# Kernel optimization log

Hardware: AMD Instinct MI355X
Metric: run time of the kernel (lower is better)

The kernel has to match this reference:

```python
import jax, jax.numpy as jnp
import numpy as np

B, S, V, E, H, MAX_OOVS = 32, 1024, 32000, 256, 512, 12
D2 = 2 * H + 100          # encoder feature dim after binary concat
IN = E + D2               # GRU input size


def setup_inputs() -> dict:
    key = jax.random.key(0)
    ks = jax.random.split(key, 18)
    sc = 0.02
    return {
        "input_idx": jax.random.randint(ks[0], (B,), 0, V),
        "encoded": jax.random.normal(ks[1], (B, S, 2 * H), jnp.float32),
        "encoded_idx": jax.random.randint(ks[2], (B, S), 0, V + MAX_OOVS),
        "prev_state": jax.random.normal(ks[3], (B, H), jnp.float32),
        "weighted": jax.random.normal(ks[4], (B, 1, D2), jnp.float32),
        "binary_vectors": jax.random.uniform(ks[5], (B, S, 1), jnp.float32),
        "order": 1,
        "embed_table": jax.random.normal(ks[6], (V, E), jnp.float32) * sc,
        "W_ih": jax.random.normal(ks[7], (3 * H, IN), jnp.float32) * sc,
        "b_ih": jax.random.normal(ks[8], (3 * H,), jnp.float32) * sc,
        "W_hh": jax.random.normal(ks[9], (3 * H, H), jnp.float32) * sc,
        "b_hh": jax.random.normal(ks[10], (3 * H,), jnp.float32) * sc,
        "Wo_w": jax.random.normal(ks[11], (V, H), jnp.float32) * sc,
        "Wo_b": jax.random.normal(ks[12], (V,), jnp.float32) * sc,
        "Wc_w": jax.random.normal(ks[13], (H, D2), jnp.float32) * sc,
        "Wc_b": jax.random.normal(ks[14], (H,), jnp.float32) * sc,
        "Ws_w": jax.random.normal(ks[15], (H, D2), jnp.float32) * sc,
        "Ws_b": jax.random.normal(ks[16], (H,), jnp.float32) * sc,
    }


def _gru_step(x, h, W_ih, b_ih, W_hh, b_hh):
    # torch nn.GRU single-step math
    gi = x @ W_ih.T + b_ih
    gh = h @ W_hh.T + b_hh
    i_r, i_z, i_n = jnp.split(gi, 3, axis=1)
    h_r, h_z, h_n = jnp.split(gh, 3, axis=1)
    r = jax.nn.sigmoid(i_r + h_r)
    z = jax.nn.sigmoid(i_z + h_z)
    n = jnp.tanh(i_n + r * h_n)
    return (1.0 - z) * n + z * h


def reference(input_idx, encoded, encoded_idx, prev_state, weighted,
              binary_vectors, order, embed_table, W_ih, b_ih, W_hh, b_hh,
              Wo_w, Wo_b, Wc_w, Wc_b, Ws_w, Ws_b):
    b, s = encoded.shape[0], encoded.shape[1]
    vocab = Wo_w.shape[0]
    # concat binary feature expanded to 100 channels -> (b, s, 2H+100)
    bin100 = jnp.broadcast_to(binary_vectors, (b, s, 100))
    enc = jnp.concatenate([encoded, bin100], axis=2)

    if order == 0:
        prev_state = enc[:, -1] @ Ws_w.T + Ws_b
        weighted = jnp.zeros((b, 1, enc.shape[2]), enc.dtype)

    emb = embed_table[input_idx][:, None, :]          # (b,1,E)
    x = jnp.concatenate([emb, weighted], axis=2)[:, 0]  # (b, IN)
    state = _gru_step(x, prev_state, W_ih, b_ih, W_hh, b_hh)  # (b,H)

    score_g = state @ Wo_w.T + Wo_b                   # (b, V)
    sc = jnp.tanh(enc @ Wc_w.T + Wc_b)                # (b, s, H)
    score_c = jnp.tanh(jnp.einsum('bsh,bh->bs', sc, state))
    score_c = score_c + jnp.where(encoded_idx == 0, -1000.0, 0.0).astype(score_c.dtype)

    probs = jax.nn.softmax(jnp.concatenate([score_g, score_c], axis=1), axis=1)
    prob_g = probs[:, :vocab]
    prob_c = probs[:, vocab:]
    prob_c_given = prob_c / jnp.sum(prob_c)           # faithful: scalar sum over all elems

    oovs = jnp.full((b, MAX_OOVS), 1e-4, probs.dtype)
    prob_g = jnp.concatenate([prob_g, oovs], axis=1)  # (b, V+OOV)

    # scatter-add copy probs into vocab space (same math as one_hot + bmm)
    rows = jnp.arange(b)[:, None]
    prob_c_to_g = jnp.zeros((b, vocab + MAX_OOVS), probs.dtype).at[rows, encoded_idx].add(prob_c)
    out = (prob_g + prob_c_to_g)[:, None, :]          # (b,1,V+OOV)

    idx_from = (encoded_idx == input_idx[:, None]).astype(probs.dtype)
    ssum = idx_from.sum(axis=1, keepdims=True)
    idx_from = jnp.where(ssum > 1, idx_from / ssum, idx_from)

    attn = prob_c_given * idx_from                    # (b, s)
    weighted_out = jnp.einsum('bs,bsd->bd', attn, enc)[:, None, :]
    return out, state, weighted_out
```

## Files before the change

kernel.cpp:

```cpp
#include <hip/hip_runtime.h>

#define B_   32
#define S_   1024
#define V_   32000
#define E_   256
#define H_   512
#define D2_  1124
#define IN_  1380
#define INP_ 1408
#define G3_  1536
#define VO_  32012
#define NKT_ 36

typedef __bf16 bf16x8 __attribute__((ext_vector_type(8)));
typedef float  f32x4  __attribute__((ext_vector_type(4)));

static __device__ __forceinline__ unsigned short f2bf(float f) {
    union { float f; unsigned int u; } v; v.f = f;
    unsigned int u = v.u;
    unsigned int r = (u + 0x7FFFu + ((u >> 16) & 1u)) >> 16;
    return (unsigned short)r;
}

static __device__ __forceinline__ unsigned int pkbf(unsigned int a, unsigned int b) {
    return ((a + 0x8000u) >> 16) | ((b + 0x8000u) & 0xffff0000u);
}

static __device__ __forceinline__ uint4 pack4(uint4 a, uint4 b) {
    uint4 o;
    o.x = pkbf(a.x, a.y); o.y = pkbf(a.z, a.w);
    o.z = pkbf(b.x, b.y); o.w = pkbf(b.z, b.w);
    return o;
}

static __device__ __forceinline__ uint4 pack_bin(unsigned int binu, int kbase) {
    unsigned int x[8];
#pragma unroll
    for (int j = 0; j < 8; j++) x[j] = (kbase + j < D2_) ? binu : 0u;
    uint4 o;
    o.x = pkbf(x[0], x[1]); o.y = pkbf(x[2], x[3]);
    o.z = pkbf(x[4], x[5]); o.w = pkbf(x[6], x[7]);
    return o;
}

static __device__ __forceinline__ float tanh_fast(float x) {
    float e = __builtin_amdgcn_exp2f(x * 2.8853901817f);
    return 1.0f - 2.0f * __builtin_amdgcn_rcpf(e + 1.0f);
}

__global__ void k_prep0(const int* order, const float* prev, const float* weighted,
                        const float* encoded, const float* bin,
                        const float* Ws_w, const float* Ws_b,
                        float* prev_eff, float* weff) {
    int b = blockIdx.x, t = threadIdx.x;
    if (order[0] != 0) {
        for (int i = t; i < H_;  i += 256) prev_eff[b * H_ + i] = prev[b * H_ + i];
        for (int i = t; i < D2_; i += 256) weff[b * D2_ + i] = weighted[b * D2_ + i];
    } else {
        for (int i = t; i < D2_; i += 256) weff[b * D2_ + i] = 0.0f;
        const float* encrow = encoded + ((size_t)(b * S_ + (S_ - 1))) * 1024;
        float bv = bin[b * S_ + (S_ - 1)];
        for (int h = t; h < H_; h += 256) {
            float acc = Ws_b[h];
            const float* wr = Ws_w + (size_t)h * D2_;
            for (int d = 0; d < 1024; d++) acc += encrow[d] * wr[d];
            for (int d = 1024; d < D2_; d++) acc += bv * wr[d];
            prev_eff[b * H_ + h] = acc;
        }
    }
}

__global__ void k_build_x(const int* input_idx, const float* embed, const float* weff, float* x) {
    int idx = blockIdx.x * 256 + threadIdx.x;
    int b = idx / INP_, d = idx % INP_;
    float v;
    if (d < E_)        v = embed[(size_t)input_idx[b] * E_ + d];
    else if (d < IN_)  v = weff[b * D2_ + (d - E_)];
    else               v = 0.0f;
    x[idx] = v;
}

__global__ void k_pack_wc(const float* Wc_w, unsigned short* bpack) {
    int idx = blockIdx.x * 256 + threadIdx.x;
    int j = idx & 7, lane = (idx >> 3) & 63, ht = (idx >> 9) & 31, kt = idx >> 14;
    int h = ht * 16 + (lane & 15);
    int k = kt * 32 + (lane >> 4) * 8 + j;
    float v = (k < D2_) ? Wc_w[(size_t)h * D2_ + k] : 0.0f;
    bpack[idx] = f2bf(v);
}

__global__ void k_gi(const float* x, const float* W_ih, const float* b_ih, float* gi) {
    extern __shared__ float smemF[];
    int t = threadIdx.x;
    int bh = blockIdx.x & 1;
    int hq = blockIdx.x >> 1;
    const float4* xg = (const float4*)(x + (size_t)bh * 16 * INP_);
    float4* xl4 = (float4*)smemF;
    for (int j = t; j < 16 * INP_ / 4; j += 256) xl4[j] = xg[j];
    __syncthreads();
    int w = t >> 6, l = t & 63;
    int h3 = hq * 4 + w;
    const float* wr = W_ih + (size_t)h3 * IN_;
    float4 wv[6];
#pragma unroll
    for (int i = 0; i < 6; i++) {
        int k = 4 * l + 256 * i;
        if (k + 3 < IN_) wv[i] = *(const float4*)(wr + k);
        else {
            float a0 = (k     < IN_) ? wr[k]     : 0.f;
            float a1 = (k + 1 < IN_) ? wr[k + 1] : 0.f;
            float a2 = (k + 2 < IN_) ? wr[k + 2] : 0.f;
            float a3 = (k + 3 < IN_) ? wr[k + 3] : 0.f;
            wv[i] = make_float4(a0, a1, a2, a3);
        }
    }
    float bias = b_ih[h3];
    for (int bb = 0; bb < 16; bb++) {
        const float4* xr = xl4 + bb * (INP_ / 4);
        float p = 0.f;
#pragma unroll
        for (int i = 0; i < 6; i++) {
            int k = 4 * l + 256 * i;
            if (k < INP_) {
                float4 xv = xr[l + 64 * i];
                p += wv[i].x * xv.x + wv[i].y * xv.y + wv[i].z * xv.z + wv[i].w * xv.w;
            }
        }
#pragma unroll
        for (int off = 32; off >= 1; off >>= 1) p += __shfl_xor(p, off, 64);
        if (l == 0) gi[(bh * 16 + bb) * G3_ + h3] = p + bias;
    }
}

__global__ void k_gh(const float* prev_eff, const float* W_hh, const float* b_hh, float* gh) {
    extern __shared__ float smemF[];
    int t = threadIdx.x;
    const float4* pg = (const float4*)prev_eff;
    float4* pl4 = (float4*)smemF;
    for (int j = t; j < B_ * H_ / 4; j += 256) pl4[j] = pg[j];
    __syncthreads();
    int w = t >> 6, l = t & 63;
    int h3 = blockIdx.x * 4 + w;
    const float* wr = W_hh + (size_t)h3 * H_;
    float4 w0 = *(const float4*)(wr + 4 * l);
    float4 w1 = *(const float4*)(wr + 256 + 4 * l);
    float bias = b_hh[h3];
    for (int bb = 0; bb < B_; bb++) {
        const float* pr = smemF + bb * H_;
        float4 s0 = *(const float4*)(pr + 4 * l);
        float4 s1 = *(const float4*)(pr + 256 + 4 * l);
        float p = w0.x * s0.x + w0.y * s0.y + w0.z * s0.z + w0.w * s0.w
                + w1.x * s1.x + w1.y * s1.y + w1.z * s1.z + w1.w * s1.w;
#pragma unroll
        for (int off = 32; off >= 1; off >>= 1) p += __shfl_xor(p, off, 64);
        if (l == 0) gh[bb * G3_ + h3] = p + bias;
    }
}

__global__ void k_gate(const float* gi, const float* gh, const float* prev_eff,
                       float* state, float* out_state) {
    int idx = blockIdx.x * 256 + threadIdx.x;
    int b = idx >> 9, h = idx & 511;
    float ir = gi[b * G3_ + h],           hr = gh[b * G3_ + h];
    float iz = gi[b * G3_ + H_ + h],      hz = gh[b * G3_ + H_ + h];
    float in_ = gi[b * G3_ + 2 * H_ + h], hn = gh[b * G3_ + 2 * H_ + h];
    float r = 1.0f / (1.0f + expf(-(ir + hr)));
    float z = 1.0f / (1.0f + expf(-(iz + hz)));
    float n = tanhf(in_ + r * hn);
    float st = (1.0f - z) * n + z * prev_eff[idx];
    state[idx] = st;
    out_state[idx] = st;
}

__global__ void __launch_bounds__(256) k_scoreg(const float* state, const float* Wo_w,
                                                const float* Wo_b, float* scoreg) {
    __shared__ unsigned short Abf[32 * 520];
    int t = threadIdx.x;
    {
        int m = t & 31, g = t >> 5;
        const float4* src = (const float4*)(state + m * 512 + g * 64);
        unsigned short* dst = &Abf[m * 520 + g * 64];
#pragma unroll
        for (int i = 0; i < 16; i++) {
            float4 v = src[i];
            ushort4 p; p.x = f2bf(v.x); p.y = f2bf(v.y); p.z = f2bf(v.z); p.w = f2bf(v.w);
            *(ushort4*)(dst + i * 4) = p;
        }
    }
    __syncthreads();
    int w = t >> 6, l = t & 63;
    int q = l >> 4, m16 = l & 15;
    int n = blockIdx.x * 64 + w * 16 + m16;
    const uint4* wrow = (const uint4*)(Wo_w + (size_t)n * 512 + q * 8);
    f32x4 acc0 = {0.f, 0.f, 0.f, 0.f}, acc1 = {0.f, 0.f, 0.f, 0.f};
#pragma unroll
    for (int kt = 0; kt < 16; kt++) {
        uint4 w0 = wrow[kt * 8];
        uint4 w1 = wrow[kt * 8 + 1];
        int4 pb;
        pb.x = (int)pkbf(w0.x, w0.y); pb.y = (int)pkbf(w0.z, w0.w);
        pb.z = (int)pkbf(w1.x, w1.y); pb.w = (int)pkbf(w1.z, w1.w);
        bf16x8 bv = *(bf16x8*)&pb;
        bf16x8 a0 = *(const bf16x8*)&Abf[m16 * 520 + kt * 32 + q * 8];
        bf16x8 a1 = *(const bf16x8*)&Abf[(16 + m16) * 520 + kt * 32 + q * 8];
        acc0 = __builtin_amdgcn_mfma_f32_16x16x32_bf16(a0, bv, acc0, 0, 0, 0);
        acc1 = __builtin_amdgcn_mfma_f32_16x16x32_bf16(a1, bv, acc1, 0, 0, 0);
    }
    float wb = Wo_b[n];
#pragma unroll
    for (int r = 0; r < 4; r++) {
        scoreg[(q * 4 + r) * V_ + n]        = acc0[r] + wb;
        scoreg[(16 + q * 4 + r) * V_ + n]   = acc1[r] + wb;
    }
}

__global__ void __launch_bounds__(256) k_sc(
    const float* encoded, const float* bin, const unsigned short* bpack,
    const float* Wc_b, const float* state, float* scorec) {
    __shared__ unsigned short Abuf[2][4096];
    __shared__ float partL[4][128];
    int t = threadIdx.x;
    int b  = blockIdx.x >> 4;
    int s0 = ((blockIdx.x >> 1) & 7) << 7;
    int hh = blockIdx.x & 1;
    int w = t >> 6, l = t & 63;
    int q = l >> 4, m = l & 15;

    int r   = t >> 1;
    int cq0 = t & 1;
    int cq1 = cq0 + 2;
    const uint4* encp = (const uint4*)(encoded + ((size_t)(b * S_ + s0 + r)) * 1024);
    unsigned int binu = __float_as_uint(bin[b * S_ + s0 + r]);
    int wro0 = r * 32 + ((cq0 ^ (r & 3)) << 3);
    int wro1 = r * 32 + ((cq1 ^ (r & 3)) << 3);

    f32x4 acc[8][4];
#pragma unroll
    for (int i = 0; i < 8; i++)
#pragma unroll
        for (int j = 0; j < 4; j++) { acc[i][j][0]=0.f; acc[i][j][1]=0.f; acc[i][j][2]=0.f; acc[i][j][3]=0.f; }

    {
        uint4 a0 = encp[cq0 * 2], a1 = encp[cq0 * 2 + 1];
        uint4 b0 = encp[cq1 * 2], b1 = encp[cq1 * 2 + 1];
        *(uint4*)&Abuf[0][wro0] = pack4(a0, a1);
        *(uint4*)&Abuf[0][wro1] = pack4(b0, b1);
    }
    const unsigned short* bvbase = bpack + ((size_t)((hh * 16 + w * 4) * 64 + l)) * 8;
    __syncthreads();
    bf16x8 bv[4];
#pragma unroll
    for (int jj = 0; jj < 4; jj++) bv[jj] = *(const bf16x8*)(bvbase + jj * 512);

#pragma unroll 2
    for (int kt = 0; kt < NKT_; kt++) {
        int cur = kt & 1;
        uint4 na0, na1, nb0, nb1;
        if (kt + 1 < 32) {
            na0 = encp[(kt + 1) * 8 + cq0 * 2]; na1 = encp[(kt + 1) * 8 + cq0 * 2 + 1];
            nb0 = encp[(kt + 1) * 8 + cq1 * 2]; nb1 = encp[(kt + 1) * 8 + cq1 * 2 + 1];
        }
        bf16x8 bvn[4];
        if (kt + 1 < NKT_) {
#pragma unroll
            for (int jj = 0; jj < 4; jj++)
                bvn[jj] = *(const bf16x8*)(bvbase + (size_t)(kt + 1) * 16384 + jj * 512);
        }
#pragma unroll
        for (int st = 0; st < 8; st++) {
            bf16x8 a = *(const bf16x8*)&Abuf[cur][(st * 16 + m) * 32 + ((q ^ (m & 3)) << 3)];
#pragma unroll
            for (int jj = 0; jj < 4; jj++)
                acc[st][jj] = __builtin_amdgcn_mfma_f32_16x16x32_bf16(a, bv[jj], acc[st][jj], 0, 0, 0);
        }
        if (kt + 1 < NKT_) {
            uint4 p0, p1;
            if (kt + 1 < 32) { p0 = pack4(na0, na1); p1 = pack4(nb0, nb1); }
            else {
                p0 = pack_bin(binu, (kt + 1) * 32 + cq0 * 8);
                p1 = pack_bin(binu, (kt + 1) * 32 + cq1 * 8);
            }
            *(uint4*)&Abuf[cur ^ 1][wro0] = p0;
            *(uint4*)&Abuf[cur ^ 1][wro1] = p1;
        }
        __syncthreads();
#pragma unroll
        for (int jj = 0; jj < 4; jj++) bv[jj] = bvn[jj];
    }

    float hb[4], hs[4];
#pragma unroll
    for (int jj = 0; jj < 4; jj++) {
        int h = (hh * 16 + w * 4 + jj) * 16 + m;
        hb[jj] = Wc_b[h];
        hs[jj] = state[b * H_ + h];
    }
#pragma unroll
    for (int st = 0; st < 8; st++) {
#pragma unroll
        for (int rr = 0; rr < 4; rr++) {
            float val = 0.f;
#pragma unroll
            for (int jj = 0; jj < 4; jj++)
                val += tanh_fast(acc[st][jj][rr] + hb[jj]) * hs[jj];
            val += __shfl_xor(val, 1, 64);
            val += __shfl_xor(val, 2, 64);
            val += __shfl_xor(val, 4, 64);
            val += __shfl_xor(val, 8, 64);
            if (m == 0) partL[w][st * 16 + q * 4 + rr] = val;
        }
    }
    __syncthreads();
    if (t < 128) {
        float tot = partL[0][t] + partL[1][t] + partL[2][t] + partL[3][t];
        atomicAdd(&scorec[b * 1024 + s0 + t], tot);
    }
}

__global__ void k_exp(float* scoreg, float* scorec, const int* enc_idx,
                      float* partA, float* partC) {
    int blk = blockIdx.x;
    int b = blk / 17, c = blk % 17;
    int t = threadIdx.x;
    float sa = 0.f;
    if (c < 16) {
        int base = b * V_ + c * 2000;
        for (int i = t; i < 2000; i += 256) {
            float e = __expf(scoreg[base + i]);
            scoreg[base + i] = e;
            sa += e;
        }
    } else {
        int base = b * 1024;
        for (int i = t; i < 1024; i += 256) {
            float v = scorec[base + i];
            float s = tanh_fast(v) + (enc_idx[base + i] == 0 ? -1000.0f : 0.0f);
            float e = __expf(s);
            scorec[base + i] = e;
            sa += e;
        }
    }
#pragma unroll
    for (int off = 32; off >= 1; off >>= 1) sa += __shfl_xor(sa, off, 64);
    __shared__ float rA[4];
    int w = t >> 6, l = t & 63;
    if (l == 0) rA[w] = sa;
    __syncthreads();
    if (t == 0) {
        float tot = rA[0] + rA[1] + rA[2] + rA[3];
        partA[blk] = tot;
        if (c == 16) partC[b] = tot;
    }
}

__global__ void k_combine(const float* partA, const float* partC, float* rowinv, float* invgc,
                          int* cnt, int* list, const int* enc_idx, const int* input_idx) {
    __shared__ float rs[32], rc[32];
    int t = threadIdx.x;
    if (t < 32) {
        float a = 0.f;
        for (int j = 0; j < 17; j++) a += partA[t * 17 + j];
        rs[t] = a; rc[t] = partC[t];
        rowinv[t] = 1.0f / a;
        cnt[t] = 0;
    }
    __syncthreads();
    if (t == 0) {
        float g = 0.f;
        for (int b = 0; b < 32; b++) g += rc[b] / rs[b];
        invgc[0] = 1.0f / g;
    }
    for (int i = t; i < B_ * S_; i += 512) {
        int b = i >> 10;
        if (enc_idx[i] == input_idx[b]) {
            int p = atomicAdd(&cnt[b], 1);
            list[b * S_ + p] = i & 1023;
        }
    }
}

__global__ void k_write(const float* scoreg, const float* scorec, const float* rowinv,
                        float* out, float* probc) {
    int idx = blockIdx.x * 256 + threadIdx.x;
    if (idx < B_ * V_) {
        int b = idx / V_, v = idx - b * V_;
        out[b * VO_ + v] = scoreg[idx] * rowinv[b];
    } else if (idx < B_ * V_ + B_ * S_) {
        int j = idx - B_ * V_;
        int b = j >> 10;
        probc[j] = scorec[j] * rowinv[b];
    } else {
        int j = idx - B_ * V_ - B_ * S_;
        if (j < B_ * 12) {
            int b = j / 12;
            out[b * VO_ + V_ + (j - b * 12)] = 0.0001f;
        }
    }
}

__global__ void k_scatter(const float* probc, const int* enc_idx, float* out) {
    int idx = blockIdx.x * 256 + threadIdx.x;
    int b = idx >> 10;
    atomicAdd(&out[b * VO_ + enc_idx[idx]], probc[idx]);
}

__global__ void k_wo(const float* probc, const int* list, const int* cnt, const float* invgc,
                     const float* encoded, const float* bin, float* out2) {
    int b = blockIdx.x, t = threadIdx.x;
    __shared__ float aL[1024];
    __shared__ int   sL[1024];
    int n = cnt[b];
    float scale = invgc[0] * (n > 1 ? 1.0f / (float)n : 1.0f);
    for (int i = t; i < n; i += 256) {
        int s = list[b * S_ + i];
        sL[i] = s;
        aL[i] = probc[b * S_ + s] * scale;
    }
    __syncthreads();
    for (int d = t; d < D2_; d += 256) {
        float acc = 0.f;
        for (int i = 0; i < n; i++) {
            int s = sL[i];
            float ev = (d < 1024) ? encoded[((size_t)(b * S_ + s)) * 1024 + d] : bin[b * S_ + s];
            acc += aL[i] * ev;
        }
        out2[b * D2_ + d] = acc;
    }
}

extern "C" void kernel_launch(void* const* d_in, const int* in_sizes, int n_in,
                              void* d_out, int out_size, void* d_ws, size_t ws_size,
                              hipStream_t stream) {
    const int*   input_idx = (const int*)d_in[0];
    const float* encoded   = (const float*)d_in[1];
    const int*   enc_idx   = (const int*)d_in[2];
    const float* prev      = (const float*)d_in[3];
    const float* weighted  = (const float*)d_in[4];
    const float* bin       = (const float*)d_in[5];
    const int*   order     = (const int*)d_in[6];
    const float* embed     = (const float*)d_in[7];
    const float* W_ih      = (const float*)d_in[8];
    const float* b_ih      = (const float*)d_in[9];
    const float* W_hh      = (const float*)d_in[10];
    const float* b_hh      = (const float*)d_in[11];
    const float* Wo_w      = (const float*)d_in[12];
    const float* Wo_b      = (const float*)d_in[13];
    const float* Wc_w      = (const float*)d_in[14];
    const float* Wc_b      = (const float*)d_in[15];
    const float* Ws_w      = (const float*)d_in[16];
    const float* Ws_b      = (const float*)d_in[17];

    float* out  = (float*)d_out;
    float* out1 = out + B_ * VO_;
    float* out2 = out1 + B_ * H_;

    float* ws_f     = (float*)d_ws;
    float* w_state  = ws_f;
    float* w_prev   = ws_f + 16384;
    float* w_weff   = ws_f + 32768;
    float* w_x      = ws_f + 68736;
    float* w_gi     = ws_f + 113792;
    float* w_gh     = ws_f + 162944;
    float* w_scoreg = ws_f + 212096;
    float* w_scorec = ws_f + 1236096;
    float* w_probc  = ws_f + 1268864;
    float* w_partA  = ws_f + 1301632;
    float* w_partC  = ws_f + 1302176;
    float* w_rowinv = ws_f + 1302208;
    float* w_invgc  = ws_f + 1302240;
    int*   w_cnt    = (int*)(ws_f + 1302248);
    int*   w_list   = w_cnt + 32;
    unsigned short* w_bpack = (unsigned short*)(ws_f + 1335048);

    k_prep0<<<32, 256, 0, stream>>>(order, prev, weighted, encoded, bin, Ws_w, Ws_b, w_prev, w_weff);
    k_build_x<<<176, 256, 0, stream>>>(input_idx, embed, w_weff, w_x);
    k_pack_wc<<<2304, 256, 0, stream>>>(Wc_w, w_bpack);
    k_gi<<<768, 256, 16 * INP_ * sizeof(float), stream>>>(w_x, W_ih, b_ih, w_gi);
    k_gh<<<384, 256, B_ * H_ * sizeof(float), stream>>>(w_prev, W_hh, b_hh, w_gh);
    k_gate<<<64, 256, 0, stream>>>(w_gi, w_gh, w_prev, w_state, out1);
    hipMemsetAsync(w_scorec, 0, B_ * S_ * sizeof(float), stream);
    k_scoreg<<<500, 256, 0, stream>>>(w_state, Wo_w, Wo_b, w_scoreg);
    k_sc<<<512, 256, 0, stream>>>(encoded, bin, w_bpack, Wc_b, w_state, w_scorec);
    k_exp<<<544, 256, 0, stream>>>(w_scoreg, w_scorec, enc_idx, w_partA, w_partC);
    k_combine<<<1, 512, 0, stream>>>(w_partA, w_partC, w_rowinv, w_invgc, w_cnt, w_list, enc_idx, input_idx);
    k_write<<<4130, 256, 0, stream>>>(w_scoreg, w_scorec, w_rowinv, out, w_probc);
    k_scatter<<<128, 256, 0, stream>>>(w_probc, enc_idx, out);
    k_wo<<<32, 256, 0, stream>>>(w_probc, w_list, w_cnt, w_invgc, encoded, bin, out2);
}
```

Before: 466.7 us.

## Retile copy-score GEMM to cover full H per block with LDS-staged weights

Each k_sc block now covers 64 sequence rows across all 512 hidden units with 512 threads, instead of 128 rows by half the hidden dim. The packed Wc weights are streamed into LDS with global_load_lds, and tanh plus the mask are applied in-kernel. This removes the atomicAdd accumulation, the scorec memset, and the tanh/mask work in k_exp. It also merges k_prep0 and k_build_x into one kernel and drops a bounds check in k_gi; the cost is a larger LDS footprint and a different occupancy profile in k_sc.

```diff
diff --git a/kernel.cpp b/kernel.cpp
--- a/kernel.cpp
+++ b/kernel.cpp
@@ -26,38 +26,35 @@
     return ((a + 0x8000u) >> 16) | ((b + 0x8000u) & 0xffff0000u);
 }
 
-static __device__ __forceinline__ uint4 pack4(uint4 a, uint4 b) {
-    uint4 o;
-    o.x = pkbf(a.x, a.y); o.y = pkbf(a.z, a.w);
-    o.z = pkbf(b.x, b.y); o.w = pkbf(b.z, b.w);
-    return o;
-}
-
-static __device__ __forceinline__ uint4 pack_bin(unsigned int binu, int kbase) {
-    unsigned int x[8];
-#pragma unroll
-    for (int j = 0; j < 8; j++) x[j] = (kbase + j < D2_) ? binu : 0u;
-    uint4 o;
-    o.x = pkbf(x[0], x[1]); o.y = pkbf(x[2], x[3]);
-    o.z = pkbf(x[4], x[5]); o.w = pkbf(x[6], x[7]);
-    return o;
-}
-
 static __device__ __forceinline__ float tanh_fast(float x) {
     float e = __builtin_amdgcn_exp2f(x * 2.8853901817f);
     return 1.0f - 2.0f * __builtin_amdgcn_rcpf(e + 1.0f);
 }
 
-__global__ void k_prep0(const int* order, const float* prev, const float* weighted,
-                        const float* encoded, const float* bin,
-                        const float* Ws_w, const float* Ws_b,
-                        float* prev_eff, float* weff) {
+static __device__ __forceinline__ void glds16(const void* g, void* l) {
+    __builtin_amdgcn_global_load_lds(
+        (const __attribute__((address_space(1))) unsigned int*)g,
+        (__attribute__((address_space(3))) unsigned int*)l, 16, 0, 0);
+}
+
+__global__ void k_prep(const int* order, const int* input_idx, const float* embed,
+                       const float* weighted, const float* prev,
+                       const float* encoded, const float* bin,
+                       const float* Ws_w, const float* Ws_b,
+                       float* x, float* prev_eff) {
     int b = blockIdx.x, t = threadIdx.x;
-    if (order[0] != 0) {
-        for (int i = t; i < H_;  i += 256) prev_eff[b * H_ + i] = prev[b * H_ + i];
-        for (int i = t; i < D2_; i += 256) weff[b * D2_ + i] = weighted[b * D2_ + i];
+    int ord = order[0];
+    const float* emb = embed + (size_t)input_idx[b] * E_;
+    for (int d = t; d < INP_; d += 256) {
+        float v;
+        if (d < E_)       v = emb[d];
+        else if (d < IN_) v = ord ? weighted[b * D2_ + (d - E_)] : 0.0f;
+        else              v = 0.0f;
+        x[b * INP_ + d] = v;
+    }
+    if (ord) {
+        for (int i = t; i < H_; i += 256) prev_eff[b * H_ + i] = prev[b * H_ + i];
     } else {
-        for (int i = t; i < D2_; i += 256) weff[b * D2_ + i] = 0.0f;
         const float* encrow = encoded + ((size_t)(b * S_ + (S_ - 1))) * 1024;
         float bv = bin[b * S_ + (S_ - 1)];
         for (int h = t; h < H_; h += 256) {
@@ -68,16 +65,6 @@
             prev_eff[b * H_ + h] = acc;
         }
     }
-}
-
-__global__ void k_build_x(const int* input_idx, const float* embed, const float* weff, float* x) {
-    int idx = blockIdx.x * 256 + threadIdx.x;
-    int b = idx / INP_, d = idx % INP_;
-    float v;
-    if (d < E_)        v = embed[(size_t)input_idx[b] * E_ + d];
-    else if (d < IN_)  v = weff[b * D2_ + (d - E_)];
-    else               v = 0.0f;
-    x[idx] = v;
 }
 
 __global__ void k_pack_wc(const float* Wc_w, unsigned short* bpack) {
@@ -120,11 +107,8 @@
         float p = 0.f;
 #pragma unroll
         for (int i = 0; i < 6; i++) {
-            int k = 4 * l + 256 * i;
-            if (k < INP_) {
-                float4 xv = xr[l + 64 * i];
-                p += wv[i].x * xv.x + wv[i].y * xv.y + wv[i].z * xv.z + wv[i].w * xv.w;
-            }
+            float4 xv = xr[l + 64 * i];
+            p += wv[i].x * xv.x + wv[i].y * xv.y + wv[i].z * xv.z + wv[i].w * xv.w;
         }
 #pragma unroll
         for (int off = 32; off >= 1; off >>= 1) p += __shfl_xor(p, off, 64);
@@ -214,111 +198,110 @@
     }
 }
 
-__global__ void __launch_bounds__(256) k_sc(
+__global__ void __launch_bounds__(512) k_sc(
     const float* encoded, const float* bin, const unsigned short* bpack,
-    const float* Wc_b, const float* state, float* scorec) {
-    __shared__ unsigned short Abuf[2][4096];
-    __shared__ float partL[4][128];
+    const float* Wc_b, const float* state, const int* enc_idx, float* scorec) {
+    __shared__ unsigned short Ab[2][2048];
+    __shared__ unsigned short Bb[2][16384];
+    __shared__ float partL[8][64];
     int t = threadIdx.x;
     int b  = blockIdx.x >> 4;
-    int s0 = ((blockIdx.x >> 1) & 7) << 7;
-    int hh = blockIdx.x & 1;
+    int s0 = (blockIdx.x & 15) << 6;
     int w = t >> 6, l = t & 63;
     int q = l >> 4, m = l & 15;
 
-    int r   = t >> 1;
-    int cq0 = t & 1;
-    int cq1 = cq0 + 2;
-    const uint4* encp = (const uint4*)(encoded + ((size_t)(b * S_ + s0 + r)) * 1024);
-    unsigned int binu = __float_as_uint(bin[b * S_ + s0 + r]);
-    int wro0 = r * 32 + ((cq0 ^ (r & 3)) << 3);
-    int wro1 = r * 32 + ((cq1 ^ (r & 3)) << 3);
-
-    f32x4 acc[8][4];
-#pragma unroll
-    for (int i = 0; i < 8; i++)
+    int ar = t >> 3, ak = (t & 7) * 4;
+    const float* encrow = encoded + ((size_t)(b * S_ + s0 + ar)) * 1024 + ak;
+    float binf = bin[b * S_ + s0 + ar];
+
+    f32x4 acc[4][4];
+#pragma unroll
+    for (int i = 0; i < 4; i++)
 #pragma unroll
         for (int j = 0; j < 4; j++) { acc[i][j][0]=0.f; acc[i][j][1]=0.f; acc[i][j][2]=0.f; acc[i][j][3]=0.f; }
 
     {
-        uint4 a0 = encp[cq0 * 2], a1 = encp[cq0 * 2 + 1];
-        uint4 b0 = encp[cq1 * 2], b1 = encp[cq1 * 2 + 1];
-        *(uint4*)&Abuf[0][wro0] = pack4(a0, a1);
-        *(uint4*)&Abuf[0][wro1] = pack4(b0, b1);
-    }
-    const unsigned short* bvbase = bpack + ((size_t)((hh * 16 + w * 4) * 64 + l)) * 8;
-    __syncthreads();
-    bf16x8 bv[4];
-#pragma unroll
-    for (int jj = 0; jj < 4; jj++) bv[jj] = *(const bf16x8*)(bvbase + jj * 512);
+        float4 a0 = *(const float4*)encrow;
+        ushort4 p; p.x = f2bf(a0.x); p.y = f2bf(a0.y); p.z = f2bf(a0.z); p.w = f2bf(a0.w);
+        *(ushort4*)&Ab[0][ar * 32 + ak] = p;
+#pragma unroll
+        for (int i = 0; i < 4; i++)
+            glds16(bpack + (size_t)((i * 8 + w) * 64 + l) * 8, &Bb[0][(i * 8 + w) * 512]);
+    }
+    float4 a1 = *(const float4*)(encrow + 32);
+    __syncthreads();
 
 #pragma unroll 2
     for (int kt = 0; kt < NKT_; kt++) {
         int cur = kt & 1;
-        uint4 na0, na1, nb0, nb1;
-        if (kt + 1 < 32) {
-            na0 = encp[(kt + 1) * 8 + cq0 * 2]; na1 = encp[(kt + 1) * 8 + cq0 * 2 + 1];
-            nb0 = encp[(kt + 1) * 8 + cq1 * 2]; nb1 = encp[(kt + 1) * 8 + cq1 * 2 + 1];
-        }
-        bf16x8 bvn[4];
         if (kt + 1 < NKT_) {
+            int nx = cur ^ 1;
+#pragma unroll
+            for (int i = 0; i < 4; i++)
+                glds16(bpack + (size_t)(kt + 1) * 16384 + (size_t)((i * 8 + w) * 64 + l) * 8,
+                       &Bb[nx][(i * 8 + w) * 512]);
+            ushort4 pn;
+            if (kt + 1 < 32) {
+                pn.x = f2bf(a1.x); pn.y = f2bf(a1.y); pn.z = f2bf(a1.z); pn.w = f2bf(a1.w);
+            } else {
+                int kb = (kt + 1) * 32 + ak;
+                pn.x = f2bf(kb     < D2_ ? binf : 0.f);
+                pn.y = f2bf(kb + 1 < D2_ ? binf : 0.f);
+                pn.z = f2bf(kb + 2 < D2_ ? binf : 0.f);
+                pn.w = f2bf(kb + 3 < D2_ ? binf : 0.f);
+            }
+            *(ushort4*)&Ab[nx][ar * 32 + ak] = pn;
+            if (kt + 2 < 32) a1 = *(const float4*)(encrow + (kt + 2) * 32);
+        }
+        bf16x8 av[4], bv[4];
+#pragma unroll
+        for (int st = 0; st < 4; st++)
+            av[st] = *(const bf16x8*)&Ab[cur][(st * 16 + m) * 32 + q * 8];
+#pragma unroll
+        for (int jj = 0; jj < 4; jj++)
+            bv[jj] = *(const bf16x8*)&Bb[cur][((w * 4 + jj) * 64 + l) * 8];
+#pragma unroll
+        for (int st = 0; st < 4; st++)
 #pragma unroll
             for (int jj = 0; jj < 4; jj++)
-                bvn[jj] = *(const bf16x8*)(bvbase + (size_t)(kt + 1) * 16384 + jj * 512);
-        }
-#pragma unroll
-        for (int st = 0; st < 8; st++) {
-            bf16x8 a = *(const bf16x8*)&Abuf[cur][(st * 16 + m) * 32 + ((q ^ (m & 3)) << 3)];
-#pragma unroll
-            for (int jj = 0; jj < 4; jj++)
-                acc[st][jj] = __builtin_amdgcn_mfma_f32_16x16x32_bf16(a, bv[jj], acc[st][jj], 0, 0, 0);
-        }
-        if (kt + 1 < NKT_) {
-            uint4 p0, p1;
-            if (kt + 1 < 32) { p0 = pack4(na0, na1); p1 = pack4(nb0, nb1); }
-            else {
-                p0 = pack_bin(binu, (kt + 1) * 32 + cq0 * 8);
-                p1 = pack_bin(binu, (kt + 1) * 32 + cq1 * 8);
-            }
-            *(uint4*)&Abuf[cur ^ 1][wro0] = p0;
-            *(uint4*)&Abuf[cur ^ 1][wro1] = p1;
-        }
+                acc[st][jj] = __builtin_amdgcn_mfma_f32_16x16x32_bf16(av[st], bv[jj], acc[st][jj], 0, 0, 0);
         __syncthreads();
-#pragma unroll
-        for (int jj = 0; jj < 4; jj++) bv[jj] = bvn[jj];
     }
 
     float hb[4], hs[4];
 #pragma unroll
     for (int jj = 0; jj < 4; jj++) {
-        int h = (hh * 16 + w * 4 + jj) * 16 + m;
+        int h = (w * 4 + jj) * 16 + m;
         hb[jj] = Wc_b[h];
         hs[jj] = state[b * H_ + h];
     }
 #pragma unroll
-    for (int st = 0; st < 8; st++) {
-#pragma unroll
-        for (int rr = 0; rr < 4; rr++) {
+    for (int st = 0; st < 4; st++) {
+#pragma unroll
+        for (int r = 0; r < 4; r++) {
             float val = 0.f;
 #pragma unroll
             for (int jj = 0; jj < 4; jj++)
-                val += tanh_fast(acc[st][jj][rr] + hb[jj]) * hs[jj];
+                val += tanh_fast(acc[st][jj][r] + hb[jj]) * hs[jj];
             val += __shfl_xor(val, 1, 64);
             val += __shfl_xor(val, 2, 64);
             val += __shfl_xor(val, 4, 64);
             val += __shfl_xor(val, 8, 64);
-            if (m == 0) partL[w][st * 16 + q * 4 + rr] = val;
-        }
-    }
-    __syncthreads();
-    if (t < 128) {
-        float tot = partL[0][t] + partL[1][t] + partL[2][t] + partL[3][t];
-        atomicAdd(&scorec[b * 1024 + s0 + t], tot);
-    }
-}
-
-__global__ void k_exp(float* scoreg, float* scorec, const int* enc_idx,
-                      float* partA, float* partC) {
+            if (m == 0) partL[w][st * 16 + q * 4 + r] = val;
+        }
+    }
+    __syncthreads();
+    if (t < 64) {
+        float tot = 0.f;
+#pragma unroll
+        for (int ww = 0; ww < 8; ww++) tot += partL[ww][t];
+        int s = s0 + t;
+        int ei = enc_idx[b * S_ + s];
+        scorec[b * S_ + s] = tanh_fast(tot) + (ei == 0 ? -1000.0f : 0.0f);
+    }
+}
+
+__global__ void k_exp(float* scoreg, float* scorec, float* partA, float* partC) {
     int blk = blockIdx.x;
     int b = blk / 17, c = blk % 17;
     int t = threadIdx.x;
@@ -333,9 +316,7 @@
     } else {
         int base = b * 1024;
         for (int i = t; i < 1024; i += 256) {
-            float v = scorec[base + i];
-            float s = tanh_fast(v) + (enc_idx[base + i] == 0 ? -1000.0f : 0.0f);
-            float e = __expf(s);
+            float e = __expf(scorec[base + i]);
             scorec[base + i] = e;
             sa += e;
         }
@@ -457,7 +438,6 @@
     float* ws_f     = (float*)d_ws;
     float* w_state  = ws_f;
     float* w_prev   = ws_f + 16384;
-    float* w_weff   = ws_f + 32768;
     float* w_x      = ws_f + 68736;
     float* w_gi     = ws_f + 113792;
     float* w_gh     = ws_f + 162944;
@@ -472,16 +452,15 @@
     int*   w_list   = w_cnt + 32;
     unsigned short* w_bpack = (unsigned short*)(ws_f + 1335048);
 
-    k_prep0<<<32, 256, 0, stream>>>(order, prev, weighted, encoded, bin, Ws_w, Ws_b, w_prev, w_weff);
-    k_build_x<<<176, 256, 0, stream>>>(input_idx, embed, w_weff, w_x);
+    k_prep<<<32, 256, 0, stream>>>(order, input_idx, embed, weighted, prev,
+                                   encoded, bin, Ws_w, Ws_b, w_x, w_prev);
     k_pack_wc<<<2304, 256, 0, stream>>>(Wc_w, w_bpack);
     k_gi<<<768, 256, 16 * INP_ * sizeof(float), stream>>>(w_x, W_ih, b_ih, w_gi);
     k_gh<<<384, 256, B_ * H_ * sizeof(float), stream>>>(w_prev, W_hh, b_hh, w_gh);
     k_gate<<<64, 256, 0, stream>>>(w_gi, w_gh, w_prev, w_state, out1);
-    hipMemsetAsync(w_scorec, 0, B_ * S_ * sizeof(float), stream);
     k_scoreg<<<500, 256, 0, stream>>>(w_state, Wo_w, Wo_b, w_scoreg);
-    k_sc<<<512, 256, 0, stream>>>(encoded, bin, w_bpack, Wc_b, w_state, w_scorec);
-    k_exp<<<544, 256, 0, stream>>>(w_scoreg, w_scorec, enc_idx, w_partA, w_partC);
+    k_sc<<<512, 512, 0, stream>>>(encoded, bin, w_bpack, Wc_b, w_state, enc_idx, w_scorec);
+    k_exp<<<544, 256, 0, stream>>>(w_scoreg, w_scorec, w_partA, w_partC);
     k_combine<<<1, 512, 0, stream>>>(w_partA, w_partC, w_rowinv, w_invgc, w_cnt, w_list, enc_idx, input_idx);
     k_write<<<4130, 256, 0, stream>>>(w_scoreg, w_scorec, w_rowinv, out, w_probc);
     k_scatter<<<128, 256, 0, stream>>>(w_probc, enc_idx, out);
```

New measurement: 440.4 us. 5.6% less time.
